# Kernel tuning notes

Measured on AMD Instinct MI355X. Metric: run time of the kernel, lower is better.

Reference implementation:

```python
import jax, jax.numpy as jnp
import numpy as np
import math

B, M, H, K, SPAN = 8, 1024, 512, 8, 1024
D = H // K
MK = M + SPAN


def _skew(X, pad_value):
    # shift every row one step to the right: [N, M, L] -> [N, M, M+L]
    N, m, L = X.shape
    X = jnp.pad(X, ((0, 0), (0, 0), (0, m + 1)), constant_values=pad_value)
    X = X.reshape(N, -1)[:, :-m]
    return X.reshape(N, m, m + L)


def _unskew(X):
    # reverse of _skew: [N, M, M+L] -> [N, M, L]
    N, m, Lk = X.shape
    L = Lk - m
    X = jnp.pad(X.reshape(N, -1), ((0, 0), (0, m)))
    return X.reshape(N, m, Lk + 1)[:, :, :L]


def setup_inputs() -> dict:
    key0 = jax.random.key(0)
    ks = jax.random.split(key0, 8)
    w_scale = 1.0 / math.sqrt(H)
    return {
        "query": jax.random.normal(ks[0], (B, M, H), jnp.float32),
        "key": jax.random.normal(ks[1], (B, MK, H), jnp.float32),
        "value": jax.random.normal(ks[2], (B, MK, H), jnp.float32),
        "pos_encoding": jax.random.normal(ks[3], (D, SPAN), jnp.float32) * w_scale,
        "Wq": jax.random.normal(ks[4], (H, H), jnp.float32) * w_scale,
        "Wk": jax.random.normal(ks[5], (H, H), jnp.float32) * w_scale,
        "Wv": jax.random.normal(ks[6], (H, H), jnp.float32) * w_scale,
        "Wo": jax.random.normal(ks[7], (H, H), jnp.float32) * w_scale,
    }


def _heads(x, W):
    # project then split heads: [B, T, H] -> [B*K, T, D]
    x = x @ W
    Bx, T, _ = x.shape
    x = x.reshape(Bx, T, K, D).transpose(0, 2, 1, 3)
    return x.reshape(Bx * K, T, D)


def reference(query, key, value, pos_encoding, Wq, Wk, Wv, Wo):
    q = _heads(query, Wq)      # [B*K, M, D]
    k = _heads(key, Wk)        # [B*K, MK, D]
    v = _heads(value, Wv)      # [B*K, MK, D]

    attn_ctx = jnp.einsum("nmd,nld->nml", q, k)   # [B*K, M, MK]
    attn_ctx = _unskew(attn_ctx)                    # [B*K, M, SPAN]
    attn_pos = jnp.einsum("nmd,ds->nms", q, pos_encoding)  # [B*K, M, SPAN]
    attn = jax.nn.softmax((attn_ctx + attn_pos) / math.sqrt(D), axis=-1)

    attn_sk = _skew(attn, 0.0)                      # [B*K, M, MK]
    out = jnp.einsum("nml,nld->nmd", attn_sk, v)   # [B*K, M, D]
    out = out.reshape(B, K, M, D).transpose(0, 2, 1, 3).reshape(B, M, H)
    return out @ Wo
```

## Files before the change

### kernel.cpp

```cpp
#include <hip/hip_runtime.h>
#include <stdint.h>

#define Bq 8
#define Mq 1024
#define Hq 512
#define NHq 8
#define Dq 64
#define SPANq 1024
#define MKq 2048
#define PR2 168

typedef __bf16 bf16x8 __attribute__((ext_vector_type(8)));
typedef _Float16 f16x8 __attribute__((ext_vector_type(8)));
typedef float f32x4 __attribute__((ext_vector_type(4)));
typedef unsigned short ushort8 __attribute__((ext_vector_type(8)));
typedef unsigned int uint2v __attribute__((ext_vector_type(2)));
typedef unsigned int uint4v __attribute__((ext_vector_type(4)));

static __device__ __forceinline__ unsigned short f2bf(float f) {
  union { float f; unsigned u; } x; x.f = f;
  unsigned r = x.u + 0x7FFFu + ((x.u >> 16) & 1u);
  return (unsigned short)(r >> 16);
}

static __device__ __forceinline__ unsigned pk_f16(float a, float b) {
  return __builtin_bit_cast(unsigned, __builtin_amdgcn_cvt_pkrtz(a, b));
}

static __device__ __forceinline__ unsigned pk_bf16(float a, float b) {
  unsigned r;
  asm("v_cvt_pk_bf16_f32 %0, %1, %2" : "=v"(r) : "v"(a), "v"(b));
  return r;
}

static __device__ __forceinline__ f32x4 mfma_bf16(bf16x8 a, bf16x8 b, f32x4 c) {
  return __builtin_amdgcn_mfma_f32_16x16x32_bf16(a, b, c, 0, 0, 0);
}
static __device__ __forceinline__ f32x4 mfma_f16(f16x8 a, f16x8 b, f32x4 c) {
  return __builtin_amdgcn_mfma_f32_16x16x32_f16(a, b, c, 0, 0, 0);
}

static __device__ __forceinline__ void async_ld16(const void* g, void* l) {
  __builtin_amdgcn_global_load_lds(
      (const __attribute__((address_space(1))) void*)g,
      (__attribute__((address_space(3))) void*)l, 16, 0, 0);
}

__global__ __launch_bounds__(256) void prep_transpose(
    const float* __restrict__ Wq, const float* __restrict__ Wk,
    const float* __restrict__ Wv, const float* __restrict__ Wo,
    const float* __restrict__ pos,
    unsigned short* __restrict__ WTq, unsigned short* __restrict__ WTk,
    unsigned short* __restrict__ WTv, unsigned short* __restrict__ WTo,
    unsigned short* __restrict__ posT) {
  __shared__ float tile[64][65];
  const int bid = blockIdx.x;
  const float* src; unsigned short* dst;
  int src_stride, dst_stride, i0, o0;
  if (bid < 256) {
    const int w = bid >> 6, t = bid & 63;
    src = (w == 0) ? Wq : (w == 1) ? Wk : (w == 2) ? Wv : Wo;
    dst = (w == 0) ? WTq : (w == 1) ? WTk : (w == 2) ? WTv : WTo;
    src_stride = Hq; dst_stride = Hq;
    i0 = (t >> 3) * 64; o0 = (t & 7) * 64;
  } else {
    const int t = bid - 256;
    src = pos; dst = posT;
    src_stride = SPANq; dst_stride = Dq;
    i0 = 0; o0 = t * 64;
  }
  const int tid = threadIdx.x;
  for (int e = tid; e < 4096; e += 256) {
    const int r = e >> 6, c = e & 63;
    tile[r][c] = src[(size_t)(i0 + r) * src_stride + o0 + c];
  }
  __syncthreads();
  for (int e = tid; e < 4096; e += 256) {
    const int r = e >> 6, c = e & 63;
    dst[(size_t)(o0 + r) * dst_stride + i0 + c] = f2bf(tile[c][r]);
  }
}

__global__ __launch_bounds__(256, 2) void gemm128(
    const unsigned short* __restrict__ Xb, const unsigned short* __restrict__ WT,
    unsigned short* __restrict__ outb, _Float16* __restrict__ outv,
    float* __restrict__ outf, int mode, int tshift) {
  __shared__ unsigned short sh[18432];
  unsigned short* As = sh;
  unsigned short* Bs = sh + 8192;
  const int tid = threadIdx.x;
  const int wave = tid >> 6, lane = tid & 63;
  const int q = lane >> 4, l16 = lane & 15;
  const int wy = wave >> 1, wx = wave & 1;
  const size_t m0 = (size_t)blockIdx.x * 128;
  const int n0 = blockIdx.y * 128;
  const int dsub = lane >> 3;
  const int dswz = (lane & 7) ^ dsub;

  f32x4 acc[4][4] = {};

  for (int k0 = 0; k0 < Hq; k0 += 64) {
    __syncthreads();
#pragma unroll
    for (int i = 0; i < 4; i++) {
      const int s = wave * 4 + i;
      const int r = s * 8 + dsub;
      async_ld16(Xb + (m0 + r) * Hq + k0 + dswz * 8, As + s * 512);
      async_ld16(WT + (size_t)(n0 + r) * Hq + k0 + dswz * 8, Bs + s * 512);
    }
    __syncthreads();
    bf16x8 af[2][4], bg[2][4];
#pragma unroll
    for (int h = 0; h < 2; h++) {
#pragma unroll
      for (int mt = 0; mt < 4; mt++) {
        const int R = wy * 64 + mt * 16 + l16;
        af[h][mt] = *(const bf16x8*)(As + R * 64 + (((h * 4 + q) ^ (l16 & 7)) * 8));
      }
#pragma unroll
      for (int nt = 0; nt < 4; nt++) {
        const int R = wx * 64 + nt * 16 + l16;
        bg[h][nt] = *(const bf16x8*)(Bs + R * 64 + (((h * 4 + q) ^ (l16 & 7)) * 8));
      }
    }
#pragma unroll
    for (int h = 0; h < 2; h++)
#pragma unroll
      for (int mt = 0; mt < 4; mt++)
#pragma unroll
        for (int nt = 0; nt < 4; nt++)
          acc[mt][nt] = mfma_bf16(af[h][mt], bg[h][nt], acc[mt][nt]);
  }

  const int Tlen = 1 << tshift;
#pragma unroll
  for (int mt = 0; mt < 4; mt++) {
#pragma unroll
    for (int nt = 0; nt < 4; nt++) {
      const int c = n0 + wx * 64 + nt * 16 + l16;
#pragma unroll
      for (int r = 0; r < 4; r++) {
        const int m = (int)m0 + wy * 64 + mt * 16 + q * 4 + r;
        const float val = acc[mt][nt][r];
        if (mode == 3) {
          outf[(size_t)m * Hq + c] = val;
        } else {
          const int b = m >> tshift, t = m & (Tlen - 1);
          const int head = c >> 6, d = c & 63;
          outb[(((size_t)(b * 8 + head) << tshift) + t) * 64 + d] = f2bf(val);
        }
      }
    }
  }
}

__global__ __launch_bounds__(256, 2) void gemm_qkv(
    const float* __restrict__ qF, const float* __restrict__ kF,
    const float* __restrict__ vF,
    const unsigned short* __restrict__ WTq, const unsigned short* __restrict__ WTk,
    const unsigned short* __restrict__ WTv,
    unsigned short* __restrict__ qb, unsigned short* __restrict__ kbuf,
    _Float16* __restrict__ vTb) {
  __shared__ float shf[12288];
  float* As = shf;
  unsigned short* Bs = (unsigned short*)(shf + 8192);

  const int x = blockIdx.x;
  const float* Xf; const unsigned short* WT;
  unsigned short* outb = nullptr; _Float16* outv = nullptr;
  int mode, tshift, bx;
  if (x < 64)       { Xf = qF; WT = WTq; outb = qb;   mode = 0; tshift = 10; bx = x; }
  else if (x < 192) { Xf = kF; WT = WTk; outb = kbuf; mode = 0; tshift = 11; bx = x - 64; }
  else              { Xf = vF; WT = WTv; outv = vTb;  mode = 2; tshift = 11; bx = x - 192; }

  const int tid = threadIdx.x;
  const int wave = tid >> 6, lane = tid & 63;
  const int q = lane >> 4, l16 = lane & 15;
  const int wy = wave >> 1, wx = wave & 1;
  const size_t m0 = (size_t)bx * 128;
  const int n0 = blockIdx.y * 128;
  const int dsub = lane >> 3;
  const int dswz = (lane & 7) ^ dsub;
  const int arow = lane >> 4;
  const int apos = lane & 15;

  f32x4 acc[4][4] = {};

  for (int k0 = 0; k0 < Hq; k0 += 64) {
    __syncthreads();
#pragma unroll
    for (int i = 0; i < 8; i++) {
      const int s = wave * 8 + i;
      const int r = s * 4 + arow;
      const int gsw = apos ^ (((s & 1) << 2) | arow);
      async_ld16(Xf + (m0 + r) * Hq + k0 + gsw * 4, As + s * 256);
    }
#pragma unroll
    for (int i = 0; i < 4; i++) {
      const int s = wave * 4 + i;
      const int r = s * 8 + dsub;
      async_ld16(WT + (size_t)(n0 + r) * Hq + k0 + dswz * 8, Bs + s * 512);
    }
    __syncthreads();

    bf16x8 af[2][4], bg[2][4];
#pragma unroll
    for (int h = 0; h < 2; h++) {
#pragma unroll
      for (int mt = 0; mt < 4; mt++) {
        const int R = wy * 64 + mt * 16 + l16;
        const int xr = R & 7;
        const int c0 = h * 8 + q * 2;
        const f32x4 a0 = *(const f32x4*)(As + R * 64 + ((c0 ^ xr) * 4));
        const f32x4 a1 = *(const f32x4*)(As + R * 64 + (((c0 + 1) ^ xr) * 4));
        uint4v w;
        w[0] = pk_bf16(a0[0], a0[1]);
        w[1] = pk_bf16(a0[2], a0[3]);
        w[2] = pk_bf16(a1[0], a1[1]);
        w[3] = pk_bf16(a1[2], a1[3]);
        af[h][mt] = __builtin_bit_cast(bf16x8, w);
      }
#pragma unroll
      for (int nt = 0; nt < 4; nt++) {
        const int R = wx * 64 + nt * 16 + l16;
        bg[h][nt] = *(const bf16x8*)(Bs + R * 64 + (((h * 4 + q) ^ (l16 & 7)) * 8));
      }
    }
#pragma unroll
    for (int h = 0; h < 2; h++)
#pragma unroll
      for (int mt = 0; mt < 4; mt++)
#pragma unroll
        for (int nt = 0; nt < 4; nt++)
          acc[mt][nt] = mfma_bf16(af[h][mt], bg[h][nt], acc[mt][nt]);
  }

  if (mode == 2) {
    __syncthreads();
    _Float16* tr = (_Float16*)shf + wave * 4608;
#pragma unroll
    for (int nt = 0; nt < 4; nt++)
#pragma unroll
      for (int mt = 0; mt < 4; mt++)
#pragma unroll
        for (int r = 0; r < 4; r++)
          tr[(nt * 16 + l16) * 72 + mt * 16 + q * 4 + r] = (_Float16)acc[mt][nt][r];
    const int head = blockIdx.y * 2 + wx;
    const int mrow0 = (int)m0 + wy * 64;
    const int Tlen = 1 << tshift;
    const int b = mrow0 >> tshift, t0 = mrow0 & (Tlen - 1);
#pragma unroll
    for (int it = 0; it < 8; it++) {
      const int dl = it * 8 + (lane >> 3), tl = (lane & 7) * 8;
      const f16x8 v = *(const f16x8*)(tr + dl * 72 + tl);
      *(f16x8*)(outv + ((size_t)((b * 8 + head) * 64 + dl)) * Tlen + t0 + tl) = v;
    }
    return;
  }

  const int Tlen = 1 << tshift;
#pragma unroll
  for (int mt = 0; mt < 4; mt++) {
#pragma unroll
    for (int nt = 0; nt < 4; nt++) {
      const int c = n0 + wx * 64 + nt * 16 + l16;
#pragma unroll
      for (int r = 0; r < 4; r++) {
        const int m = (int)m0 + wy * 64 + mt * 16 + q * 4 + r;
        const int b = m >> tshift, t = m & (Tlen - 1);
        const int head = c >> 6, d = c & 63;
        outb[(((size_t)(b * 8 + head) << tshift) + t) * 64 + d] = f2bf(acc[mt][nt][r]);
      }
    }
  }
}

__global__ __launch_bounds__(256, 2) void attn3(
    const unsigned short* __restrict__ qb, const unsigned short* __restrict__ kglob,
    const _Float16* __restrict__ vT, const unsigned short* __restrict__ posT,
    unsigned short* __restrict__ ctx) {
  __shared__ unsigned short Kt[12288];
  __shared__ unsigned short Pt[8192];
  __shared__ unsigned short Psh[4 * 16 * PR2];

  const int tid = threadIdx.x;
  const int wave = tid >> 6, lane = tid & 63;
  const int q = lane >> 4, l16 = lane & 15;
  const int n = blockIdx.y;
  const int m0 = blockIdx.x * 64;
  const int m0w = m0 + wave * 16;
  const int dsub = lane >> 3;
  const int dswz = (lane & 7) ^ dsub;

  unsigned short* row = Psh + (wave * 16 + l16) * PR2;

  const unsigned short* qbase = qb + ((size_t)n * Mq + m0w + l16) * Dq;
  const bf16x8 qf0 = *(const bf16x8*)(qbase + q * 8);
  const bf16x8 qf1 = *(const bf16x8*)(qbase + 32 + q * 8);

  const unsigned short* kbn = kglob + (size_t)n * MKq * Dq;
  const _Float16* vbn = vT + (size_t)n * Dq * MKq;

  f32x4 O[4] = {};
  float zrow = 0.f, mrow = -1e30f;

  for (int c = 0; c < 8; c++) {
    const int sbase = c * 128;
    const int jb = m0 + sbase;
    const int j00 = m0w + sbase;

    __syncthreads();
#pragma unroll
    for (int i = 0; i < 6; i++) {
      const int s = wave + 4 * i;
      const int r = s * 8 + dsub;
      async_ld16(kbn + (size_t)(jb + r) * Dq + dswz * 8, Kt + s * 512);
    }
#pragma unroll
    for (int i = 0; i < 4; i++) {
      const int s = wave + 4 * i;
      const int r = s * 8 + dsub;
      async_ld16(posT + (size_t)(sbase + r) * Dq + dswz * 8, Pt + s * 512);
    }
    __syncthreads();

#pragma unroll
    for (int t = 0; t < 8; t++) {
      const int rl = t * 16 + l16;
      const int ch = (q ^ (l16 & 7)) * 8;
      const bf16x8 p0 = *(const bf16x8*)(Pt + rl * 64 + ch);
      const bf16x8 p1 = *(const bf16x8*)(Pt + rl * 64 + (ch ^ 32));
      f32x4 b = {};
      b = mfma_bf16(p0, qf0, b);
      b = mfma_bf16(p1, qf1, b);
      const int cw = 16 + t * 16 + 4 * q + l16;
      row[cw + 0] = f2bf(b[0]);
      row[cw + 1] = f2bf(b[1]);
      row[cw + 2] = f2bf(b[2]);
      row[cw + 3] = f2bf(b[3]);
    }

    f32x4 S[9];
#pragma unroll
    for (int t = 0; t < 9; t++) {
      const int rl = wave * 16 + t * 16 + l16;
      const int ch = (q ^ (l16 & 7)) * 8;
      const bf16x8 k0 = *(const bf16x8*)(Kt + rl * 64 + ch);
      const bf16x8 k1 = *(const bf16x8*)(Kt + rl * 64 + (ch ^ 32));
      f32x4 a = {};
      a = mfma_bf16(k0, qf0, a);
      a = mfma_bf16(k1, qf1, a);
      const uint2v pv = *(const uint2v*)(row + 16 + t * 16 + 4 * q);
      a[0] += __uint_as_float(pv.x << 16);
      a[1] += __uint_as_float(pv.x & 0xffff0000u);
      a[2] += __uint_as_float(pv.y << 16);
      a[3] += __uint_as_float(pv.y & 0xffff0000u);
      S[t] = a;
    }
#pragma unroll
    for (int r = 0; r < 4; r++) {
      if (4 * q + r < l16) S[0][r] = -1e30f;
      if (4 * q + r >= l16) S[8][r] = -1e30f;
    }

    float mx = -1e30f;
#pragma unroll
    for (int t = 0; t < 9; t++)
      mx = fmaxf(mx, fmaxf(fmaxf(S[t][0], S[t][1]), fmaxf(S[t][2], S[t][3])));
    mx = fmaxf(mx, __shfl_xor(mx, 16, 64));
    mx = fmaxf(mx, __shfl_xor(mx, 32, 64));
    const float m_new = fmaxf(mrow, mx);
    const float alpha = __expf((mrow - m_new) * 0.125f);
    float zs = 0.f;
#pragma unroll
    for (int t = 0; t < 9; t++) {
#pragma unroll
      for (int r = 0; r < 4; r++) {
        const float e = __expf((S[t][r] - m_new) * 0.125f);
        S[t][r] = e; zs += e;
      }
    }
    zs += __shfl_xor(zs, 16, 64);
    zs += __shfl_xor(zs, 32, 64);
    zrow = zrow * alpha + zs;
    mrow = m_new;
#pragma unroll
    for (int dt = 0; dt < 4; dt++) O[dt] *= alpha;

#pragma unroll
    for (int t = 0; t < 9; t++) {
      *(unsigned*)(row + t * 16 + 4 * q) = pk_f16(S[t][0], S[t][1]);
      *(unsigned*)(row + t * 16 + 4 * q + 2) = pk_f16(S[t][2], S[t][3]);
    }
    *(unsigned*)(row + 144 + 4 * q) = 0u;
    *(unsigned*)(row + 144 + 4 * q + 2) = 0u;

    f16x8 Bf[5];
#pragma unroll
    for (int kt = 0; kt < 5; kt++)
      Bf[kt] = *(const f16x8*)(row + kt * 32 + q * 8);
    f16x8 Vv[5][4];
#pragma unroll
    for (int kt = 0; kt < 5; kt++) {
      int j = j00 + kt * 32 + q * 8;
      if (j > MKq - 8) j = MKq - 8;
#pragma unroll
      for (int dt = 0; dt < 4; dt++)
        Vv[kt][dt] = *(const f16x8*)(vbn + (size_t)(dt * 16 + l16) * MKq + j);
    }
#pragma unroll
    for (int kt = 0; kt < 5; kt++)
#pragma unroll
      for (int dt = 0; dt < 4; dt++)
        O[dt] = mfma_f16(Vv[kt][dt], Bf[kt], O[dt]);
  }

  const float zi = 1.f / zrow;
  unsigned short* cp = ctx + ((size_t)(n >> 3) * Mq + m0w + l16) * Hq + (n & 7) * Dq;
#pragma unroll
  for (int dt = 0; dt < 4; dt++)
#pragma unroll
    for (int r = 0; r < 4; r++)
      cp[dt * 16 + q * 4 + r] = f2bf(O[dt][r] * zi);
}

extern "C" void kernel_launch(void* const* d_in, const int* in_sizes, int n_in,
                              void* d_out, int out_size, void* d_ws, size_t ws_size,
                              hipStream_t stream) {
  const float* query = (const float*)d_in[0];
  const float* key   = (const float*)d_in[1];
  const float* value = (const float*)d_in[2];
  const float* pos   = (const float*)d_in[3];
  const float* Wq    = (const float*)d_in[4];
  const float* Wk    = (const float*)d_in[5];
  const float* Wv    = (const float*)d_in[6];
  const float* Wo    = (const float*)d_in[7];
  float* out = (float*)d_out;

  char* w = (char*)d_ws;
  unsigned short* qb   = (unsigned short*)w; w += (size_t)64 * Mq * Dq * 2;
  unsigned short* kbuf = (unsigned short*)w; w += (size_t)64 * MKq * Dq * 2;
  _Float16*       vTb  = (_Float16*)w;       w += (size_t)64 * Dq * MKq * 2;
  unsigned short* posT = (unsigned short*)w; w += (size_t)SPANq * Dq * 2;
  unsigned short* WTq  = (unsigned short*)w; w += (size_t)Hq * Hq * 2;
  unsigned short* WTk  = (unsigned short*)w; w += (size_t)Hq * Hq * 2;
  unsigned short* WTv  = (unsigned short*)w; w += (size_t)Hq * Hq * 2;
  unsigned short* WTo  = (unsigned short*)w; w += (size_t)Hq * Hq * 2;
  unsigned short* ctx  = (unsigned short*)w; w += (size_t)Bq * Mq * Hq * 2;

  prep_transpose<<<272, 256, 0, stream>>>(Wq, Wk, Wv, Wo, pos, WTq, WTk, WTv, WTo, posT);
  gemm_qkv<<<dim3(320, 4), 256, 0, stream>>>(query, key, value, WTq, WTk, WTv, qb, kbuf, vTb);
  attn3<<<dim3(16, 64), 256, 0, stream>>>(qb, kbuf, vTb, posT, ctx);
  gemm128<<<dim3(64, 4), 256, 0, stream>>>(ctx, WTo, nullptr, nullptr, out, 3, 10);
}
```

Before: 276.8 us.

## Double-buffer K tile in LDS and prefetch pos and V into registers

The attention kernel now keeps two LDS buffers for the K tile. It issues the async copy of the next chunk's K while computing on the current one, which removes one of the two block barriers per iteration. The positional-encoding tile is no longer staged through LDS; each lane loads its pos fragments straight from global into registers. The V fragments are loaded at the top of the iteration so their latency overlaps the score computation. In exchange, the kernel uses more LDS per block and many more live registers (pos, V and score fragments), which risks spills or lower occupancy. It also relies on the barrier waiting for the outstanding async loads.

```diff
diff --git a/kernel.cpp b/kernel.cpp
--- a/kernel.cpp
+++ b/kernel.cpp
@@ -279,8 +279,7 @@
     const unsigned short* __restrict__ qb, const unsigned short* __restrict__ kglob,
     const _Float16* __restrict__ vT, const unsigned short* __restrict__ posT,
     unsigned short* __restrict__ ctx) {
-  __shared__ unsigned short Kt[12288];
-  __shared__ unsigned short Pt[8192];
+  __shared__ unsigned short Kt[2][12288];
   __shared__ unsigned short Psh[4 * 16 * PR2];
 
   const int tid = threadIdx.x;
@@ -304,35 +303,68 @@
   f32x4 O[4] = {};
   float zrow = 0.f, mrow = -1e30f;
 
+#pragma unroll
+  for (int i = 0; i < 6; i++) {
+    const int s = wave + 4 * i;
+    const int r = s * 8 + dsub;
+    async_ld16(kbn + (size_t)(m0 + r) * Dq + dswz * 8, &Kt[0][s * 512]);
+  }
+
   for (int c = 0; c < 8; c++) {
     const int sbase = c * 128;
-    const int jb = m0 + sbase;
     const int j00 = m0w + sbase;
 
     __syncthreads();
-#pragma unroll
-    for (int i = 0; i < 6; i++) {
-      const int s = wave + 4 * i;
-      const int r = s * 8 + dsub;
-      async_ld16(kbn + (size_t)(jb + r) * Dq + dswz * 8, Kt + s * 512);
-    }
-#pragma unroll
-    for (int i = 0; i < 4; i++) {
-      const int s = wave + 4 * i;
-      const int r = s * 8 + dsub;
-      async_ld16(posT + (size_t)(sbase + r) * Dq + dswz * 8, Pt + s * 512);
-    }
-    __syncthreads();
-
+
+    bf16x8 pf0[8], pf1[8];
 #pragma unroll
     for (int t = 0; t < 8; t++) {
-      const int rl = t * 16 + l16;
+      const unsigned short* pp = posT + (size_t)(sbase + t * 16 + l16) * Dq + q * 8;
+      pf0[t] = *(const bf16x8*)(pp);
+      pf1[t] = *(const bf16x8*)(pp + 32);
+    }
+    f16x8 Vv[5][4];
+#pragma unroll
+    for (int kt = 0; kt < 5; kt++) {
+      int j = j00 + kt * 32 + q * 8;
+      if (j > MKq - 8) j = MKq - 8;
+#pragma unroll
+      for (int dt = 0; dt < 4; dt++)
+        Vv[kt][dt] = *(const f16x8*)(vbn + (size_t)(dt * 16 + l16) * MKq + j);
+    }
+    __builtin_amdgcn_sched_barrier(0);
+
+    if (c < 7) {
+      const int jb = m0 + sbase + 128;
+      unsigned short* kd = Kt[(c + 1) & 1];
+#pragma unroll
+      for (int i = 0; i < 6; i++) {
+        const int s = wave + 4 * i;
+        const int r = s * 8 + dsub;
+        async_ld16(kbn + (size_t)(jb + r) * Dq + dswz * 8, kd + s * 512);
+      }
+    }
+
+    const unsigned short* Kc = Kt[c & 1];
+
+    f32x4 S[9];
+#pragma unroll
+    for (int t = 0; t < 9; t++) {
+      const int rl = wave * 16 + t * 16 + l16;
       const int ch = (q ^ (l16 & 7)) * 8;
-      const bf16x8 p0 = *(const bf16x8*)(Pt + rl * 64 + ch);
-      const bf16x8 p1 = *(const bf16x8*)(Pt + rl * 64 + (ch ^ 32));
+      const bf16x8 k0 = *(const bf16x8*)(Kc + rl * 64 + ch);
+      const bf16x8 k1 = *(const bf16x8*)(Kc + rl * 64 + (ch ^ 32));
+      f32x4 a = {};
+      a = mfma_bf16(k0, qf0, a);
+      a = mfma_bf16(k1, qf1, a);
+      S[t] = a;
+    }
+
+#pragma unroll
+    for (int t = 0; t < 8; t++) {
       f32x4 b = {};
-      b = mfma_bf16(p0, qf0, b);
-      b = mfma_bf16(p1, qf1, b);
+      b = mfma_bf16(pf0[t], qf0, b);
+      b = mfma_bf16(pf1[t], qf1, b);
       const int cw = 16 + t * 16 + 4 * q + l16;
       row[cw + 0] = f2bf(b[0]);
       row[cw + 1] = f2bf(b[1]);
@@ -340,22 +372,13 @@
       row[cw + 3] = f2bf(b[3]);
     }
 
-    f32x4 S[9];
 #pragma unroll
     for (int t = 0; t < 9; t++) {
-      const int rl = wave * 16 + t * 16 + l16;
-      const int ch = (q ^ (l16 & 7)) * 8;
-      const bf16x8 k0 = *(const bf16x8*)(Kt + rl * 64 + ch);
-      const bf16x8 k1 = *(const bf16x8*)(Kt + rl * 64 + (ch ^ 32));
-      f32x4 a = {};
-      a = mfma_bf16(k0, qf0, a);
-      a = mfma_bf16(k1, qf1, a);
       const uint2v pv = *(const uint2v*)(row + 16 + t * 16 + 4 * q);
-      a[0] += __uint_as_float(pv.x << 16);
-      a[1] += __uint_as_float(pv.x & 0xffff0000u);
-      a[2] += __uint_as_float(pv.y << 16);
-      a[3] += __uint_as_float(pv.y & 0xffff0000u);
-      S[t] = a;
+      S[t][0] += __uint_as_float(pv.x << 16);
+      S[t][1] += __uint_as_float(pv.x & 0xffff0000u);
+      S[t][2] += __uint_as_float(pv.y << 16);
+      S[t][3] += __uint_as_float(pv.y & 0xffff0000u);
     }
 #pragma unroll
     for (int r = 0; r < 4; r++) {
@@ -399,15 +422,6 @@
 #pragma unroll
     for (int kt = 0; kt < 5; kt++)
       Bf[kt] = *(const f16x8*)(row + kt * 32 + q * 8);
-    f16x8 Vv[5][4];
-#pragma unroll
-    for (int kt = 0; kt < 5; kt++) {
-      int j = j00 + kt * 32 + q * 8;
-      if (j > MKq - 8) j = MKq - 8;
-#pragma unroll
-      for (int dt = 0; dt < 4; dt++)
-        Vv[kt][dt] = *(const f16x8*)(vbn + (size_t)(dt * 16 + l16) * MKq + j);
-    }
 #pragma unroll
     for (int kt = 0; kt < 5; kt++)
 #pragma unroll
```

New measurement: 345.7 us. +24.9%, slower.

## Enlarge attention blocks to 8 waves and swizzle GEMM block order

Applied to the files above, without the earlier changes.

The attention kernel now runs 512 threads per block covering 128 query rows, so each K and position tile loaded into shared memory is shared by twice as many waves. This cuts redundant global loads of the K window overlap and of the positional table. The QKV and output GEMMs move to a 1-D grid with a grouped block order (8 row tiles by 4 column tiles), aiming for better L2 reuse of the weight and input tiles. The larger attention block raises LDS use and halves the block count, which may lower occupancy and latency hiding.

```diff
diff --git a/kernel.cpp b/kernel.cpp
--- a/kernel.cpp
+++ b/kernel.cpp
@@ -83,8 +83,7 @@
 
 __global__ __launch_bounds__(256, 2) void gemm128(
     const unsigned short* __restrict__ Xb, const unsigned short* __restrict__ WT,
-    unsigned short* __restrict__ outb, _Float16* __restrict__ outv,
-    float* __restrict__ outf, int mode, int tshift) {
+    float* __restrict__ outf) {
   __shared__ unsigned short sh[18432];
   unsigned short* As = sh;
   unsigned short* Bs = sh + 8192;
@@ -92,8 +91,11 @@
   const int wave = tid >> 6, lane = tid & 63;
   const int q = lane >> 4, l16 = lane & 15;
   const int wy = wave >> 1, wx = wave & 1;
-  const size_t m0 = (size_t)blockIdx.x * 128;
-  const int n0 = blockIdx.y * 128;
+  const int h = blockIdx.x;
+  const int j8 = h & 7, rr = h >> 3;
+  const int y = rr & 3, xg = rr >> 2;
+  const size_t m0 = (size_t)(xg * 8 + j8) * 128;
+  const int n0 = y * 128;
   const int dsub = lane >> 3;
   const int dswz = (lane & 7) ^ dsub;
 
@@ -111,28 +113,27 @@
     __syncthreads();
     bf16x8 af[2][4], bg[2][4];
 #pragma unroll
-    for (int h = 0; h < 2; h++) {
+    for (int hh = 0; hh < 2; hh++) {
 #pragma unroll
       for (int mt = 0; mt < 4; mt++) {
         const int R = wy * 64 + mt * 16 + l16;
-        af[h][mt] = *(const bf16x8*)(As + R * 64 + (((h * 4 + q) ^ (l16 & 7)) * 8));
+        af[hh][mt] = *(const bf16x8*)(As + R * 64 + (((hh * 4 + q) ^ (l16 & 7)) * 8));
       }
 #pragma unroll
       for (int nt = 0; nt < 4; nt++) {
         const int R = wx * 64 + nt * 16 + l16;
-        bg[h][nt] = *(const bf16x8*)(Bs + R * 64 + (((h * 4 + q) ^ (l16 & 7)) * 8));
-      }
-    }
-#pragma unroll
-    for (int h = 0; h < 2; h++)
+        bg[hh][nt] = *(const bf16x8*)(Bs + R * 64 + (((hh * 4 + q) ^ (l16 & 7)) * 8));
+      }
+    }
+#pragma unroll
+    for (int hh = 0; hh < 2; hh++)
 #pragma unroll
       for (int mt = 0; mt < 4; mt++)
 #pragma unroll
         for (int nt = 0; nt < 4; nt++)
-          acc[mt][nt] = mfma_bf16(af[h][mt], bg[h][nt], acc[mt][nt]);
-  }
-
-  const int Tlen = 1 << tshift;
+          acc[mt][nt] = mfma_bf16(af[hh][mt], bg[hh][nt], acc[mt][nt]);
+  }
+
 #pragma unroll
   for (int mt = 0; mt < 4; mt++) {
 #pragma unroll
@@ -141,14 +142,7 @@
 #pragma unroll
       for (int r = 0; r < 4; r++) {
         const int m = (int)m0 + wy * 64 + mt * 16 + q * 4 + r;
-        const float val = acc[mt][nt][r];
-        if (mode == 3) {
-          outf[(size_t)m * Hq + c] = val;
-        } else {
-          const int b = m >> tshift, t = m & (Tlen - 1);
-          const int head = c >> 6, d = c & 63;
-          outb[(((size_t)(b * 8 + head) << tshift) + t) * 64 + d] = f2bf(val);
-        }
+        outf[(size_t)m * Hq + c] = acc[mt][nt][r];
       }
     }
   }
@@ -165,7 +159,12 @@
   float* As = shf;
   unsigned short* Bs = (unsigned short*)(shf + 8192);
 
-  const int x = blockIdx.x;
+  const int h = blockIdx.x;
+  const int j8 = h & 7, rr = h >> 3;
+  const int y = rr & 3, xg = rr >> 2;
+  const int x = xg * 8 + j8;
+  const int n0 = y * 128;
+
   const float* Xf; const unsigned short* WT;
   unsigned short* outb = nullptr; _Float16* outv = nullptr;
   int mode, tshift, bx;
@@ -178,7 +177,6 @@
   const int q = lane >> 4, l16 = lane & 15;
   const int wy = wave >> 1, wx = wave & 1;
   const size_t m0 = (size_t)bx * 128;
-  const int n0 = blockIdx.y * 128;
   const int dsub = lane >> 3;
   const int dswz = (lane & 7) ^ dsub;
   const int arow = lane >> 4;
@@ -205,12 +203,12 @@
 
     bf16x8 af[2][4], bg[2][4];
 #pragma unroll
-    for (int h = 0; h < 2; h++) {
+    for (int hh = 0; hh < 2; hh++) {
 #pragma unroll
       for (int mt = 0; mt < 4; mt++) {
         const int R = wy * 64 + mt * 16 + l16;
         const int xr = R & 7;
-        const int c0 = h * 8 + q * 2;
+        const int c0 = hh * 8 + q * 2;
         const f32x4 a0 = *(const f32x4*)(As + R * 64 + ((c0 ^ xr) * 4));
         const f32x4 a1 = *(const f32x4*)(As + R * 64 + (((c0 + 1) ^ xr) * 4));
         uint4v w;
@@ -218,21 +216,21 @@
         w[1] = pk_bf16(a0[2], a0[3]);
         w[2] = pk_bf16(a1[0], a1[1]);
         w[3] = pk_bf16(a1[2], a1[3]);
-        af[h][mt] = __builtin_bit_cast(bf16x8, w);
+        af[hh][mt] = __builtin_bit_cast(bf16x8, w);
       }
 #pragma unroll
       for (int nt = 0; nt < 4; nt++) {
         const int R = wx * 64 + nt * 16 + l16;
-        bg[h][nt] = *(const bf16x8*)(Bs + R * 64 + (((h * 4 + q) ^ (l16 & 7)) * 8));
-      }
-    }
-#pragma unroll
-    for (int h = 0; h < 2; h++)
+        bg[hh][nt] = *(const bf16x8*)(Bs + R * 64 + (((hh * 4 + q) ^ (l16 & 7)) * 8));
+      }
+    }
+#pragma unroll
+    for (int hh = 0; hh < 2; hh++)
 #pragma unroll
       for (int mt = 0; mt < 4; mt++)
 #pragma unroll
         for (int nt = 0; nt < 4; nt++)
-          acc[mt][nt] = mfma_bf16(af[h][mt], bg[h][nt], acc[mt][nt]);
+          acc[mt][nt] = mfma_bf16(af[hh][mt], bg[hh][nt], acc[mt][nt]);
   }
 
   if (mode == 2) {
@@ -245,7 +243,7 @@
 #pragma unroll
         for (int r = 0; r < 4; r++)
           tr[(nt * 16 + l16) * 72 + mt * 16 + q * 4 + r] = (_Float16)acc[mt][nt][r];
-    const int head = blockIdx.y * 2 + wx;
+    const int head = y * 2 + wx;
     const int mrow0 = (int)m0 + wy * 64;
     const int Tlen = 1 << tshift;
     const int b = mrow0 >> tshift, t0 = mrow0 & (Tlen - 1);
@@ -275,19 +273,19 @@
   }
 }
 
-__global__ __launch_bounds__(256, 2) void attn3(
+__global__ __launch_bounds__(512, 1) void attn3(
     const unsigned short* __restrict__ qb, const unsigned short* __restrict__ kglob,
     const _Float16* __restrict__ vT, const unsigned short* __restrict__ posT,
     unsigned short* __restrict__ ctx) {
-  __shared__ unsigned short Kt[12288];
+  __shared__ unsigned short Kt[16384];
   __shared__ unsigned short Pt[8192];
-  __shared__ unsigned short Psh[4 * 16 * PR2];
+  __shared__ unsigned short Psh[8 * 16 * PR2];
 
   const int tid = threadIdx.x;
   const int wave = tid >> 6, lane = tid & 63;
   const int q = lane >> 4, l16 = lane & 15;
   const int n = blockIdx.y;
-  const int m0 = blockIdx.x * 64;
+  const int m0 = blockIdx.x * 128;
   const int m0w = m0 + wave * 16;
   const int dsub = lane >> 3;
   const int dswz = (lane & 7) ^ dsub;
@@ -311,14 +309,14 @@
 
     __syncthreads();
 #pragma unroll
-    for (int i = 0; i < 6; i++) {
-      const int s = wave + 4 * i;
+    for (int i = 0; i < 4; i++) {
+      const int s = wave + 8 * i;
       const int r = s * 8 + dsub;
       async_ld16(kbn + (size_t)(jb + r) * Dq + dswz * 8, Kt + s * 512);
     }
 #pragma unroll
-    for (int i = 0; i < 4; i++) {
-      const int s = wave + 4 * i;
+    for (int i = 0; i < 2; i++) {
+      const int s = wave + 8 * i;
       const int r = s * 8 + dsub;
       async_ld16(posT + (size_t)(sbase + r) * Dq + dswz * 8, Pt + s * 512);
     }
@@ -449,7 +447,7 @@
   unsigned short* ctx  = (unsigned short*)w; w += (size_t)Bq * Mq * Hq * 2;
 
   prep_transpose<<<272, 256, 0, stream>>>(Wq, Wk, Wv, Wo, pos, WTq, WTk, WTv, WTo, posT);
-  gemm_qkv<<<dim3(320, 4), 256, 0, stream>>>(query, key, value, WTq, WTk, WTv, qb, kbuf, vTb);
-  attn3<<<dim3(16, 64), 256, 0, stream>>>(qb, kbuf, vTb, posT, ctx);
-  gemm128<<<dim3(64, 4), 256, 0, stream>>>(ctx, WTo, nullptr, nullptr, out, 3, 10);
-}
+  gemm_qkv<<<1280, 256, 0, stream>>>(query, key, value, WTq, WTk, WTv, qb, kbuf, vTb);
+  attn3<<<dim3(8, 64), 512, 0, stream>>>(qb, kbuf, vTb, posT, ctx);
+  gemm128<<<256, 256, 0, stream>>>(ctx, WTo, out);
+}
```

New measurement: 265.3 us. -4.2%, faster.
